# Performance work log

Hardware: AMD Instinct MI355X
Metric: run time of the kernel (lower is better)

Reference implementation:

```python
import jax, jax.numpy as jnp
import numpy as np

B, T, D, NH, DK = 2, 2048, 1024, 16, 64
EPS = 1e-6

def proj_H(z):
    return z - z.mean(axis=-1, keepdims=True)

def to_clr(p):
    return proj_H(jnp.log(p + EPS))

def setup_inputs() -> dict:
    key = jax.random.key(0)
    ks = jax.random.split(key, 9)
    p = jax.random.uniform(ks[0], (B, T, D), dtype=jnp.float32)
    # xavier_uniform with gain=0.8 for square-ish [in,out] matrices
    def xavier(k, fan_in, fan_out):
        bound = 0.8 * np.sqrt(6.0 / (fan_in + fan_out))
        return jax.random.uniform(k, (fan_in, fan_out), minval=-bound, maxval=bound, dtype=jnp.float32)
    H = NH * DK
    Wq = xavier(ks[1], D, H); bq = jnp.zeros((H,), jnp.float32)
    Wk = xavier(ks[2], D, H); bk = jnp.zeros((H,), jnp.float32)
    Wv = xavier(ks[3], D, H); bv = jnp.zeros((H,), jnp.float32)
    Wo = xavier(ks[4], H, D); bo = jnp.zeros((D,), jnp.float32)
    return {"p": p, "Wq": Wq, "bq": bq, "Wk": Wk, "bk": bk,
            "Wv": Wv, "bv": bv, "Wo": Wo, "bo": bo}

def reference(p, Wq, bq, Wk, bk, Wv, bv, Wo, bo):
    z = to_clr(p)                                   # [B,T,D]
    # projections with H-projection epilogue, reshaped to [B,T,NH,DK]
    q = proj_H(z @ Wq + bq).reshape(B, T, NH, DK)
    k = proj_H(z @ Wk + bk).reshape(B, T, NH, DK)
    v = proj_H(z @ Wv + bv).reshape(B, T, NH, DK)
    att = jnp.einsum('bihd,bjhd->bhij', q, k) / jnp.sqrt(jnp.float32(DK))
    w = jax.nn.softmax(att, axis=-1)                # dropout is identity in eval
    z_out = jnp.einsum('bhij,bjhd->bihd', w, v).reshape(B, T, NH * DK)
    z_out = proj_H(z_out @ Wo + bo)
    return jax.nn.softmax(z_out, axis=-1)           # from_clr
```

## Files before the change

### kernel.cpp

```cpp
#include <hip/hip_runtime.h>

typedef unsigned short u16;
typedef __attribute__((ext_vector_type(8))) short short8_t;
typedef __attribute__((ext_vector_type(4))) float f32x4;
typedef __attribute__((ext_vector_type(16))) float f32x16;
typedef __attribute__((ext_vector_type(4))) int int4v;
typedef __attribute__((ext_vector_type(2))) int int2v;

#define BB    2
#define TT    2048
#define DD    1024
#define NHEAD 16
#define DKH   64
#define HH    1024
#define MR    4096
#define CLR_EPS 1e-6f
#define QSCALE_CONST 0.18033688011112042f

#define O_WQKVT  0ull
#define O_WOT    6291456ull
#define O_WMEAN  8388608ull
#define O_BQKV   8404992ull
#define O_BO     8417280ull
#define O_Z      8421376ull
#define O_QKV    16809984ull
#define O_VT     41975808ull
#define O_ZOUT   50364416ull
#define O_LOGITS O_QKV

__device__ __forceinline__ u16 f2bf(float f) {
  unsigned u = __builtin_bit_cast(unsigned, f);
  u += 0x7FFFu + ((u >> 16) & 1u);
  return (u16)(u >> 16);
}
__device__ __forceinline__ float bf2f(u16 x) {
  unsigned u = ((unsigned)x) << 16;
  return __builtin_bit_cast(float, u);
}

typedef const __attribute__((address_space(1))) unsigned int as1_u32_t;
typedef __attribute__((address_space(3))) unsigned int as3_u32_t;

__device__ __forceinline__ void async16(const void* g, void* l) {
  __builtin_amdgcn_global_load_lds((as1_u32_t*)g, (as3_u32_t*)l, 16, 0, 0);
}

__global__ __launch_bounds__(256) void wprep_mean(
    const float* __restrict__ Wq, const float* __restrict__ Wk,
    const float* __restrict__ Wv, const float* __restrict__ Wo,
    const float* __restrict__ bq, const float* __restrict__ bk,
    const float* __restrict__ bv, const float* __restrict__ bo,
    float* __restrict__ wmean, float* __restrict__ bqkv_p, float* __restrict__ bo_p) {
  __shared__ float sb[4];
  const int bid = blockIdx.x, tid = threadIdx.x;
  if (bid < 4096) {
    const int m = bid >> 10, d = bid & 1023;
    const float* Wm = (m == 0) ? Wq : (m == 1) ? Wk : (m == 2) ? Wv : Wo;
    float4 x = ((const float4*)(Wm + (size_t)d * 1024))[tid];
    float s = x.x + x.y + x.z + x.w;
    #pragma unroll
    for (int dd = 32; dd; dd >>= 1) s += __shfl_xor(s, dd);
    if ((tid & 63) == 0) sb[tid >> 6] = s;
    __syncthreads();
    if (tid == 0) wmean[bid] = (sb[0] + sb[1] + sb[2] + sb[3]) * (1.f / 1024.f);
  } else {
    const int j = bid - 4096;
    const float* bb = (j == 0) ? bq : (j == 1) ? bk : (j == 2) ? bv : bo;
    float4 x = ((const float4*)bb)[tid];
    float s = x.x + x.y + x.z + x.w;
    #pragma unroll
    for (int dd = 32; dd; dd >>= 1) s += __shfl_xor(s, dd);
    if ((tid & 63) == 0) sb[tid >> 6] = s;
    __syncthreads();
    const float mean = (sb[0] + sb[1] + sb[2] + sb[3]) * (1.f / 1024.f);
    float* dst = (j < 3) ? (bqkv_p + j * 1024) : bo_p;
    float4 o = {x.x - mean, x.y - mean, x.z - mean, x.w - mean};
    ((float4*)dst)[tid] = o;
  }
}

__global__ __launch_bounds__(256) void wprep_trans(
    const float* __restrict__ Wq, const float* __restrict__ Wk,
    const float* __restrict__ Wv, const float* __restrict__ Wo,
    const float* __restrict__ wmean, u16* __restrict__ wqkvt, u16* __restrict__ wot) {
  __shared__ float tl[64][65];
  const int tj = blockIdx.x, ti = blockIdx.y, m = blockIdx.z;
  const int tid = threadIdx.x;
  const float* Wm = (m == 0) ? Wq : (m == 1) ? Wk : (m == 2) ? Wv : Wo;
  const int d0 = ti * 64, h0 = tj * 64;
  #pragma unroll
  for (int rr = 0; rr < 4; ++rr) {
    const int r = (tid >> 4) + rr * 16;
    float4 x = *(const float4*)(Wm + (size_t)(d0 + r) * 1024 + h0 + ((tid & 15) << 2));
    const float mu = wmean[m * 1024 + d0 + r];
    tl[r][(tid & 15) * 4 + 0] = x.x - mu;
    tl[r][(tid & 15) * 4 + 1] = x.y - mu;
    tl[r][(tid & 15) * 4 + 2] = x.z - mu;
    tl[r][(tid & 15) * 4 + 3] = x.w - mu;
  }
  __syncthreads();
  #pragma unroll
  for (int rr = 0; rr < 2; ++rr) {
    const int hh = (tid >> 3) + rr * 32;
    const int cd = (tid & 7) << 3;
    short8_t v;
    #pragma unroll
    for (int i = 0; i < 8; ++i) v[i] = (short)f2bf(tl[cd + i][hh]);
    u16* dst = (m < 3) ? (wqkvt + ((size_t)(m * 1024 + h0 + hh)) * 1024 + d0 + cd)
                       : (wot + ((size_t)(h0 + hh)) * 1024 + d0 + cd);
    *(short8_t*)dst = v;
  }
}

__global__ __launch_bounds__(256) void clr_kernel(const float* __restrict__ p, u16* __restrict__ z) {
  __shared__ float sb[4];
  const int r = blockIdx.x, tid = threadIdx.x;
  float4 x = ((const float4*)(p + (size_t)r * 1024))[tid];
  float l0 = __logf(x.x + CLR_EPS), l1 = __logf(x.y + CLR_EPS);
  float l2 = __logf(x.z + CLR_EPS), l3 = __logf(x.w + CLR_EPS);
  float s = l0 + l1 + l2 + l3;
  #pragma unroll
  for (int dd = 32; dd; dd >>= 1) s += __shfl_xor(s, dd);
  if ((tid & 63) == 0) sb[tid >> 6] = s;
  __syncthreads();
  const float mu = (sb[0] + sb[1] + sb[2] + sb[3]) * (1.f / 1024.f);
  ushort4 o;
  o.x = f2bf(l0 - mu); o.y = f2bf(l1 - mu); o.z = f2bf(l2 - mu); o.w = f2bf(l3 - mu);
  ((ushort4*)(z + (size_t)r * 1024))[tid] = o;
}

template <bool OUTF32, bool QSC>
__global__ __launch_bounds__(256) void gemm_bt(
    const u16* __restrict__ A, const u16* __restrict__ Bt, const float* __restrict__ bias,
    void* __restrict__ Cout, int Ndim, int Kdim) {
  __shared__ u16 As[128 * 64];
  __shared__ u16 Bs[128 * 64];
  const int tid = threadIdx.x;
  const int lane = tid & 63, wid = tid >> 6;
  const int m0 = blockIdx.y * 128, n0 = blockIdx.x * 128;
  const int wm = wid >> 1, wn = wid & 1;
  const int srow = tid >> 3, schk = tid & 7;
  f32x4 acc[4][4] = {};

  for (int k0 = 0; k0 < Kdim; k0 += 64) {
    __syncthreads();
    #pragma unroll
    for (int rr = 0; rr < 4; ++rr) {
      const int row = srow + rr * 32;
      const int gcol = k0 + ((schk ^ (row & 7)) << 3);
      async16(A + (size_t)(m0 + row) * Kdim + gcol, &As[row * 64 + schk * 8]);
      async16(Bt + (size_t)(n0 + row) * Kdim + gcol, &Bs[row * 64 + schk * 8]);
    }
    __syncthreads();
    #pragma unroll
    for (int kk = 0; kk < 64; kk += 32) {
      short8_t af[4], bf[4];
      #pragma unroll
      for (int i = 0; i < 4; ++i) {
        const int arow = wm * 64 + i * 16 + (lane & 15);
        const int abyte = (arow * 128 + ((kk + ((lane >> 4) << 3)) << 1)) ^ ((arow & 7) << 4);
        af[i] = *(const short8_t*)((const char*)As + abyte);
        const int brow = wn * 64 + i * 16 + (lane & 15);
        const int bbyte = (brow * 128 + ((kk + ((lane >> 4) << 3)) << 1)) ^ ((brow & 7) << 4);
        bf[i] = *(const short8_t*)((const char*)Bs + bbyte);
      }
      #pragma unroll
      for (int i = 0; i < 4; ++i)
        #pragma unroll
        for (int j = 0; j < 4; ++j)
          acc[i][j] = __builtin_amdgcn_mfma_f32_16x16x32_bf16(af[i], bf[j], acc[i][j], 0, 0, 0);
    }
  }
  #pragma unroll
  for (int j = 0; j < 4; ++j) {
    const int col = n0 + wn * 64 + j * 16 + (lane & 15);
    const float bb = bias[col];
    const float sc = (QSC && col < 1024) ? QSCALE_CONST : 1.0f;
    #pragma unroll
    for (int i = 0; i < 4; ++i) {
      const int rowb = m0 + wm * 64 + i * 16 + ((lane >> 4) << 2);
      #pragma unroll
      for (int r = 0; r < 4; ++r) {
        const float v = (acc[i][j][r] + bb) * sc;
        if (OUTF32) ((float*)Cout)[(size_t)(rowb + r) * Ndim + col] = v;
        else        ((u16*)Cout)[(size_t)(rowb + r) * Ndim + col] = f2bf(v);
      }
    }
  }
}

__global__ __launch_bounds__(256) void vtrans(const u16* __restrict__ qkv, u16* __restrict__ vt) {
  __shared__ u16 tile[64][72];
  const int tt = blockIdx.x, h = blockIdx.y, b = blockIdx.z;
  const int tid = threadIdx.x;
  #pragma unroll
  for (int rr = 0; rr < 2; ++rr) {
    const int row = (tid >> 3) + rr * 32;
    const u16* src = qkv + (size_t)(b * TT + tt * 64 + row) * 3072 + 2048 + h * 64 + ((tid & 7) << 3);
    *(short8_t*)&tile[row][(tid & 7) << 3] = *(const short8_t*)src;
  }
  __syncthreads();
  #pragma unroll
  for (int rr = 0; rr < 2; ++rr) {
    const int dk = (tid >> 3) + rr * 32;
    const int t0 = (tid & 7) << 3;
    short8_t v;
    #pragma unroll
    for (int i = 0; i < 8; ++i) v[i] = (short)tile[t0 + i][dk];
    u16* dst = vt + ((size_t)(b * NHEAD + h) * 64 + dk) * (size_t)TT + tt * 64 + t0;
    *(short8_t*)dst = v;
  }
}

__global__ __launch_bounds__(512, 2) void attn_kernel(
    const u16* __restrict__ qkv, const u16* __restrict__ vt, u16* __restrict__ zout) {
  __shared__ char smem[65536];
  const int qb = blockIdx.x, h = blockIdx.y, b = blockIdx.z;
  const int tid = threadIdx.x, lane = tid & 63, w = tid >> 6;
  const int qw = w & 3, ks = w >> 2;
  const int hl = lane >> 5, l31 = lane & 31;
  const int swz = (l31 & 7) << 4;
  const int q0 = qb * 256 + qw * 64;

  short8_t qf[2][4];
  #pragma unroll
  for (int qt = 0; qt < 2; ++qt)
    #pragma unroll
    for (int c = 0; c < 4; ++c)
      qf[qt][c] = *(const short8_t*)(qkv + (size_t)(b * TT + q0 + qt * 32 + l31) * 3072
                                     + h * 64 + c * 16 + hl * 8);

  const int sr0 = qw * 16 + (lane >> 3);
  const int schk = lane & 7;
  const int scol = (schk ^ (sr0 & 7)) << 3;
  const int dof = sr0 * 128 + schk * 16;
  char* kls = smem + ks * 16384;
  char* vls = smem + 32768 + ks * 16384;
  const u16* kg = qkv + 1024 + (size_t)h * 64;
  const u16* vg = vt + (size_t)(b * NHEAD + h) * 64 * (size_t)TT;

  {
    const int kbase = ks * 1024;
    async16(kg + (size_t)(b * TT + kbase + sr0) * 3072 + scol, kls + dof);
    async16(kg + (size_t)(b * TT + kbase + sr0 + 8) * 3072 + scol, kls + dof + 1024);
    async16(vg + (size_t)sr0 * TT + kbase + scol, vls + dof);
    async16(vg + (size_t)(sr0 + 8) * TT + kbase + scol, vls + dof + 1024);
  }

  f32x16 o[2][2] = {};
  f32x16 lb[2] = {};
  short8_t ones;
  #pragma unroll
  for (int i = 0; i < 8; ++i) ones[i] = (short)0x3F80;

  for (int it = 0; it < 16; ++it) {
    __syncthreads();
    if (it < 15) {
      const int kbase = ks * 1024 + (it + 1) * 64;
      const int bo = ((it + 1) & 1) * 8192;
      async16(kg + (size_t)(b * TT + kbase + sr0) * 3072 + scol, kls + bo + dof);
      async16(kg + (size_t)(b * TT + kbase + sr0 + 8) * 3072 + scol, kls + bo + dof + 1024);
      async16(vg + (size_t)sr0 * TT + kbase + scol, vls + bo + dof);
      async16(vg + (size_t)(sr0 + 8) * TT + kbase + scol, vls + bo + dof + 1024);
    }
    const char* Kb = kls + (it & 1) * 8192;
    const char* Vb = vls + (it & 1) * 8192;

    #pragma unroll
    for (int kt = 0; kt < 2; ++kt) {
      f32x16 s[2] = {};
      #pragma unroll
      for (int c = 0; c < 4; ++c) {
        const int krow = kt * 32 + l31;
        const short8_t kfr = *(const short8_t*)(Kb + krow * 128 + ((c * 32 + hl * 16) ^ swz));
        s[0] = __builtin_amdgcn_mfma_f32_32x32x16_bf16(kfr, qf[0][c], s[0], 0, 0, 0);
        s[1] = __builtin_amdgcn_mfma_f32_32x32x16_bf16(kfr, qf[1][c], s[1], 0, 0, 0);
      }
      #pragma unroll
      for (int qt = 0; qt < 2; ++qt)
        #pragma unroll
        for (int r = 0; r < 16; ++r) {
          float pv;
          asm("v_exp_f32 %0, %1" : "=v"(pv) : "v"(s[qt][r]));
          s[qt][r] = pv;
        }
      #pragma unroll
      for (int cc = 0; cc < 2; ++cc) {
        short8_t pa[2];
        #pragma unroll
        for (int qt = 0; qt < 2; ++qt) {
          int w0, w1, w2, w3;
          asm("v_cvt_pk_bf16_f32 %0, %1, %2" : "=v"(w0) : "v"(s[qt][8 * cc + 0]), "v"(s[qt][8 * cc + 1]));
          asm("v_cvt_pk_bf16_f32 %0, %1, %2" : "=v"(w1) : "v"(s[qt][8 * cc + 2]), "v"(s[qt][8 * cc + 3]));
          asm("v_cvt_pk_bf16_f32 %0, %1, %2" : "=v"(w2) : "v"(s[qt][8 * cc + 4]), "v"(s[qt][8 * cc + 5]));
          asm("v_cvt_pk_bf16_f32 %0, %1, %2" : "=v"(w3) : "v"(s[qt][8 * cc + 6]), "v"(s[qt][8 * cc + 7]));
          int4v fw = {w0, w1, w2, w3};
          pa[qt] = __builtin_bit_cast(short8_t, fw);
          lb[qt] = __builtin_amdgcn_mfma_f32_32x32x16_bf16(pa[qt], ones, lb[qt], 0, 0, 0);
        }
        const int cb0 = 64 * kt + 32 * cc + 8 * hl;
        #pragma unroll
        for (int dkt = 0; dkt < 2; ++dkt) {
          const int vrow = dkt * 32 + l31;
          const int2v d0 = *(const int2v*)(Vb + vrow * 128 + (cb0 ^ swz));
          const int2v d1 = *(const int2v*)(Vb + vrow * 128 + ((cb0 + 16) ^ swz));
          int4v vv = {d0.x, d0.y, d1.x, d1.y};
          const short8_t vfr = __builtin_bit_cast(short8_t, vv);
          o[0][dkt] = __builtin_amdgcn_mfma_f32_32x32x16_bf16(pa[0], vfr, o[0][dkt], 0, 0, 0);
          o[1][dkt] = __builtin_amdgcn_mfma_f32_32x32x16_bf16(pa[1], vfr, o[1][dkt], 0, 0, 0);
        }
      }
    }
  }

  __syncthreads();
  const int slot = qw * 64 + lane;
  if (ks == 1) {
    u16* ro = (u16*)(smem + slot * 136);
    #pragma unroll
    for (int qt = 0; qt < 2; ++qt)
      #pragma unroll
      for (int dkt = 0; dkt < 2; ++dkt)
        #pragma unroll
        for (int r = 0; r < 16; ++r)
          ro[(qt * 2 + dkt) * 16 + r] = f2bf(o[qt][dkt][r]);
    u16* rl = (u16*)(smem + 36864 + slot * 72);
    #pragma unroll
    for (int qt = 0; qt < 2; ++qt)
      #pragma unroll
      for (int r = 0; r < 16; ++r)
        rl[qt * 16 + r] = f2bf(lb[qt][r]);
  }
  __syncthreads();
  if (ks == 0) {
    const u16* ro = (const u16*)(smem + slot * 136);
    const u16* rl = (const u16*)(smem + 36864 + slot * 72);
    #pragma unroll
    for (int qt = 0; qt < 2; ++qt) {
      #pragma unroll
      for (int r = 0; r < 16; ++r) lb[qt][r] += bf2f(rl[qt * 16 + r]);
      #pragma unroll
      for (int dkt = 0; dkt < 2; ++dkt)
        #pragma unroll
        for (int r = 0; r < 16; ++r) o[qt][dkt][r] += bf2f(ro[(qt * 2 + dkt) * 16 + r]);
    }
    #pragma unroll
    for (int qt = 0; qt < 2; ++qt) {
      float rlv[16];
      #pragma unroll
      for (int r = 0; r < 16; ++r) rlv[r] = 1.f / lb[qt][r];
      #pragma unroll
      for (int dkt = 0; dkt < 2; ++dkt) {
        const int col = h * 64 + dkt * 32 + l31;
        #pragma unroll
        for (int r = 0; r < 16; ++r) {
          const int rowg = b * TT + q0 + qt * 32 + (r & 3) + 8 * (r >> 2) + 4 * hl;
          zout[(size_t)rowg * 1024 + col] = f2bf(o[qt][dkt][r] * rlv[r]);
        }
      }
    }
  }
}

__global__ __launch_bounds__(256) void softmax_rows(const float* __restrict__ logits,
                                                    float* __restrict__ out) {
  __shared__ float sb[8];
  const int r = blockIdx.x, tid = threadIdx.x;
  float4 x = ((const float4*)(logits + (size_t)r * 1024))[tid];
  float mx = fmaxf(fmaxf(x.x, x.y), fmaxf(x.z, x.w));
  #pragma unroll
  for (int dd = 32; dd; dd >>= 1) mx = fmaxf(mx, __shfl_xor(mx, dd));
  if ((tid & 63) == 0) sb[tid >> 6] = mx;
  __syncthreads();
  mx = fmaxf(fmaxf(sb[0], sb[1]), fmaxf(sb[2], sb[3]));
  const float e0 = __expf(x.x - mx), e1 = __expf(x.y - mx);
  const float e2 = __expf(x.z - mx), e3 = __expf(x.w - mx);
  float s = e0 + e1 + e2 + e3;
  #pragma unroll
  for (int dd = 32; dd; dd >>= 1) s += __shfl_xor(s, dd);
  __syncthreads();
  if ((tid & 63) == 0) sb[4 + (tid >> 6)] = s;
  __syncthreads();
  s = sb[4] + sb[5] + sb[6] + sb[7];
  const float inv = 1.f / s;
  float4 o = {e0 * inv, e1 * inv, e2 * inv, e3 * inv};
  ((float4*)(out + (size_t)r * 1024))[tid] = o;
}

extern "C" void kernel_launch(void* const* d_in, const int* in_sizes, int n_in,
                              void* d_out, int out_size, void* d_ws, size_t ws_size,
                              hipStream_t stream) {
  (void)in_sizes; (void)n_in; (void)out_size; (void)ws_size;
  const float* p  = (const float*)d_in[0];
  const float* Wq = (const float*)d_in[1];
  const float* bq = (const float*)d_in[2];
  const float* Wk = (const float*)d_in[3];
  const float* bk = (const float*)d_in[4];
  const float* Wv = (const float*)d_in[5];
  const float* bv = (const float*)d_in[6];
  const float* Wo = (const float*)d_in[7];
  const float* bo = (const float*)d_in[8];
  float* out = (float*)d_out;

  char* ws = (char*)d_ws;
  u16*   wqkvt  = (u16*)(ws + O_WQKVT);
  u16*   wot    = (u16*)(ws + O_WOT);
  float* wmean  = (float*)(ws + O_WMEAN);
  float* bqkv_p = (float*)(ws + O_BQKV);
  float* bo_p   = (float*)(ws + O_BO);
  u16*   z      = (u16*)(ws + O_Z);
  u16*   qkv    = (u16*)(ws + O_QKV);
  u16*   vt     = (u16*)(ws + O_VT);
  u16*   zoutb  = (u16*)(ws + O_ZOUT);
  float* logits = (float*)(ws + O_LOGITS);

  wprep_mean<<<4100, 256, 0, stream>>>(Wq, Wk, Wv, Wo, bq, bk, bv, bo, wmean, bqkv_p, bo_p);
  wprep_trans<<<dim3(16, 16, 4), 256, 0, stream>>>(Wq, Wk, Wv, Wo, wmean, wqkvt, wot);
  clr_kernel<<<MR, 256, 0, stream>>>(p, z);
  gemm_bt<false, true><<<dim3(3072 / 128, MR / 128), 256, 0, stream>>>(z, wqkvt, bqkv_p, qkv, 3072, 1024);
  vtrans<<<dim3(TT / 64, NHEAD, BB), 256, 0, stream>>>(qkv, vt);
  attn_kernel<<<dim3(TT / 256, NHEAD, BB), 512, 0, stream>>>(qkv, vt, zoutb);
  gemm_bt<true, false><<<dim3(1024 / 128, MR / 128), 256, 0, stream>>>(zoutb, wot, bo_p, logits, 1024, 1024);
  softmax_rows<<<MR, 256, 0, stream>>>(logits, out);
}
```

Baseline: 139.4 us.

## Replace QKV GEMM with 256x256 double-buffered phased kernel and fuse V transpose

```diff
diff --git a/kernel.cpp b/kernel.cpp
--- a/kernel.cpp
+++ b/kernel.cpp
@@ -43,6 +43,19 @@
 
 __device__ __forceinline__ void async16(const void* g, void* l) {
   __builtin_amdgcn_global_load_lds((as1_u32_t*)g, (as3_u32_t*)l, 16, 0, 0);
+}
+
+__device__ __forceinline__ void stage2(const u16* __restrict__ G, int base_row,
+                                       int r0, int r1, int k0, int schk, u16* lds) {
+  const int c0 = k0 + ((schk ^ (r0 & 7)) << 3);
+  const int c1 = k0 + ((schk ^ (r1 & 7)) << 3);
+  async16(G + (size_t)(base_row + r0) * 1024 + c0, lds + r0 * 64 + schk * 8);
+  async16(G + (size_t)(base_row + r1) * 1024 + c1, lds + r1 * 64 + schk * 8);
+}
+
+__device__ __forceinline__ short8_t ldfrag(const u16* buf, int row, int kh, int lane) {
+  const int byte = (row * 128 + ((kh * 32 + ((lane >> 4) << 3)) << 1)) ^ ((row & 7) << 4);
+  return *(const short8_t*)((const char*)buf + byte);
 }
 
 __global__ __launch_bounds__(256) void wprep_mean(
@@ -129,10 +142,143 @@
   ((ushort4*)(z + (size_t)r * 1024))[tid] = o;
 }
 
-template <bool OUTF32, bool QSC>
+__global__ __launch_bounds__(512, 2) void gemm_qkv_8ph(
+    const u16* __restrict__ A, const u16* __restrict__ Bt, const float* __restrict__ bias,
+    u16* __restrict__ qkv, u16* __restrict__ vt) {
+  __shared__ u16 As[2][256 * 64];
+  __shared__ u16 Bs[2][256 * 64];
+  const int tid = threadIdx.x, lane = tid & 63, wid = tid >> 6;
+  const int wm = wid >> 2, wn = wid & 3;
+  const int id = blockIdx.x;
+  const int nid = (id & 7) * 24 + (id >> 3);
+  const int m0 = (nid / 12) * 256, n0 = (nid % 12) * 256;
+  const int srow = tid >> 3, schk = tid & 7;
+  const int l15 = lane & 15, lg4 = (lane >> 4) << 2;
+
+  f32x4 acc[8][4] = {};
+
+  stage2(Bt, n0, srow, srow + 64, 0, schk, &Bs[0][0]);
+  stage2(Bt, n0, srow + 128, srow + 192, 0, schk, &Bs[0][0]);
+  stage2(A, m0, srow, srow + 128, 0, schk, &As[0][0]);
+  stage2(A, m0, srow + 64, srow + 192, 0, schk, &As[0][0]);
+  asm volatile("s_waitcnt vmcnt(2)" ::: "memory");
+  __builtin_amdgcn_s_barrier();
+
+  short8_t afr[4], bfr[4];
+  for (int t = 0; t < 16; ++t) {
+    const int cur = t & 1;
+    const int k0n = ((t + 1) & 15) * 64;
+    const u16* Ab = &As[cur][0];
+    const u16* Bb_ = &Bs[cur][0];
+    u16* Asn = &As[cur ^ 1][0];
+    u16* Bsn = &Bs[cur ^ 1][0];
+
+    #pragma unroll
+    for (int j = 0; j < 4; ++j) bfr[j] = ldfrag(Bb_, wn * 64 + j * 16 + l15, 0, lane);
+    #pragma unroll
+    for (int i = 0; i < 4; ++i) afr[i] = ldfrag(Ab, wm * 128 + i * 16 + l15, 0, lane);
+    stage2(Bt, n0, srow, srow + 64, k0n, schk, Bsn);
+    asm volatile("s_waitcnt vmcnt(2)" ::: "memory");
+    __builtin_amdgcn_s_barrier();
+    asm volatile("s_waitcnt lgkmcnt(0)" ::: "memory");
+    __builtin_amdgcn_sched_barrier(0);
+    __builtin_amdgcn_s_setprio(1);
+    #pragma unroll
+    for (int i = 0; i < 4; ++i)
+      #pragma unroll
+      for (int j = 0; j < 4; ++j)
+        acc[i][j] = __builtin_amdgcn_mfma_f32_16x16x32_bf16(afr[i], bfr[j], acc[i][j], 0, 0, 0);
+    __builtin_amdgcn_s_setprio(0);
+    __builtin_amdgcn_s_barrier();
+
+    #pragma unroll
+    for (int i = 0; i < 4; ++i) afr[i] = ldfrag(Ab, wm * 128 + 64 + i * 16 + l15, 0, lane);
+    stage2(Bt, n0, srow + 128, srow + 192, k0n, schk, Bsn);
+    __builtin_amdgcn_s_barrier();
+    asm volatile("s_waitcnt lgkmcnt(0)" ::: "memory");
+    __builtin_amdgcn_sched_barrier(0);
+    __builtin_amdgcn_s_setprio(1);
+    #pragma unroll
+    for (int i = 0; i < 4; ++i)
+      #pragma unroll
+      for (int j = 0; j < 4; ++j)
+        acc[4 + i][j] = __builtin_amdgcn_mfma_f32_16x16x32_bf16(afr[i], bfr[j], acc[4 + i][j], 0, 0, 0);
+    __builtin_amdgcn_s_setprio(0);
+    __builtin_amdgcn_s_barrier();
+
+    #pragma unroll
+    for (int j = 0; j < 4; ++j) bfr[j] = ldfrag(Bb_, wn * 64 + j * 16 + l15, 1, lane);
+    #pragma unroll
+    for (int i = 0; i < 4; ++i) afr[i] = ldfrag(Ab, wm * 128 + i * 16 + l15, 1, lane);
+    stage2(A, m0, srow, srow + 128, k0n, schk, Asn);
+    __builtin_amdgcn_s_barrier();
+    asm volatile("s_waitcnt lgkmcnt(0)" ::: "memory");
+    __builtin_amdgcn_sched_barrier(0);
+    __builtin_amdgcn_s_setprio(1);
+    #pragma unroll
+    for (int i = 0; i < 4; ++i)
+      #pragma unroll
+      for (int j = 0; j < 4; ++j)
+        acc[i][j] = __builtin_amdgcn_mfma_f32_16x16x32_bf16(afr[i], bfr[j], acc[i][j], 0, 0, 0);
+    __builtin_amdgcn_s_setprio(0);
+    __builtin_amdgcn_s_barrier();
+
+    #pragma unroll
+    for (int i = 0; i < 4; ++i) afr[i] = ldfrag(Ab, wm * 128 + 64 + i * 16 + l15, 1, lane);
+    stage2(A, m0, srow + 64, srow + 192, k0n, schk, Asn);
+    asm volatile("s_waitcnt vmcnt(2)" ::: "memory");
+    __builtin_amdgcn_s_barrier();
+    asm volatile("s_waitcnt lgkmcnt(0)" ::: "memory");
+    __builtin_amdgcn_sched_barrier(0);
+    __builtin_amdgcn_s_setprio(1);
+    #pragma unroll
+    for (int i = 0; i < 4; ++i)
+      #pragma unroll
+      for (int j = 0; j < 4; ++j)
+        acc[4 + i][j] = __builtin_amdgcn_mfma_f32_16x16x32_bf16(afr[i], bfr[j], acc[4 + i][j], 0, 0, 0);
+    __builtin_amdgcn_s_setprio(0);
+    __builtin_amdgcn_s_barrier();
+  }
+  asm volatile("s_waitcnt vmcnt(0)" ::: "memory");
+
+  if (n0 < 2048) {
+    const float sc = (n0 < 1024) ? QSCALE_CONST : 1.0f;
+    #pragma unroll
+    for (int j = 0; j < 4; ++j) {
+      const int col = n0 + wn * 64 + j * 16 + l15;
+      const float bb = bias[col];
+      #pragma unroll
+      for (int i = 0; i < 8; ++i) {
+        const int rowb = m0 + wm * 128 + i * 16 + lg4;
+        #pragma unroll
+        for (int r = 0; r < 4; ++r)
+          qkv[(size_t)(rowb + r) * 3072 + col] = f2bf((acc[i][j][r] + bb) * sc);
+      }
+    }
+  } else {
+    const int h = (n0 - 2048 + wn * 64) >> 6;
+    #pragma unroll
+    for (int j = 0; j < 4; ++j) {
+      const int dk = j * 16 + l15;
+      const float bb = bias[n0 + wn * 64 + dk];
+      #pragma unroll
+      for (int i = 0; i < 8; ++i) {
+        const int rowb = m0 + wm * 128 + i * 16 + lg4;
+        const int b = rowb >> 11, tq = rowb & 2047;
+        ushort4 pk;
+        pk.x = f2bf(acc[i][j][0] + bb);
+        pk.y = f2bf(acc[i][j][1] + bb);
+        pk.z = f2bf(acc[i][j][2] + bb);
+        pk.w = f2bf(acc[i][j][3] + bb);
+        *(ushort4*)(vt + ((size_t)((b * NHEAD + h) * 64 + dk)) * TT + tq) = pk;
+      }
+    }
+  }
+}
+
 __global__ __launch_bounds__(256) void gemm_bt(
     const u16* __restrict__ A, const u16* __restrict__ Bt, const float* __restrict__ bias,
-    void* __restrict__ Cout, int Ndim, int Kdim) {
+    float* __restrict__ Cout, int Ndim, int Kdim) {
   __shared__ u16 As[128 * 64];
   __shared__ u16 Bs[128 * 64];
   const int tid = threadIdx.x;
@@ -153,16 +299,12 @@
     }
     __syncthreads();
     #pragma unroll
-    for (int kk = 0; kk < 64; kk += 32) {
+    for (int kk = 0; kk < 2; ++kk) {
       short8_t af[4], bf[4];
       #pragma unroll
       for (int i = 0; i < 4; ++i) {
-        const int arow = wm * 64 + i * 16 + (lane & 15);
-        const int abyte = (arow * 128 + ((kk + ((lane >> 4) << 3)) << 1)) ^ ((arow & 7) << 4);
-        af[i] = *(const short8_t*)((const char*)As + abyte);
-        const int brow = wn * 64 + i * 16 + (lane & 15);
-        const int bbyte = (brow * 128 + ((kk + ((lane >> 4) << 3)) << 1)) ^ ((brow & 7) << 4);
-        bf[i] = *(const short8_t*)((const char*)Bs + bbyte);
+        af[i] = ldfrag(As, wm * 64 + i * 16 + (lane & 15), kk, lane);
+        bf[i] = ldfrag(Bs, wn * 64 + i * 16 + (lane & 15), kk, lane);
       }
       #pragma unroll
       for (int i = 0; i < 4; ++i)
@@ -175,40 +317,13 @@
   for (int j = 0; j < 4; ++j) {
     const int col = n0 + wn * 64 + j * 16 + (lane & 15);
     const float bb = bias[col];
-    const float sc = (QSC && col < 1024) ? QSCALE_CONST : 1.0f;
     #pragma unroll
     for (int i = 0; i < 4; ++i) {
       const int rowb = m0 + wm * 64 + i * 16 + ((lane >> 4) << 2);
       #pragma unroll
-      for (int r = 0; r < 4; ++r) {
-        const float v = (acc[i][j][r] + bb) * sc;
-        if (OUTF32) ((float*)Cout)[(size_t)(rowb + r) * Ndim + col] = v;
-        else        ((u16*)Cout)[(size_t)(rowb + r) * Ndim + col] = f2bf(v);
-      }
-    }
-  }
-}
-
-__global__ __launch_bounds__(256) void vtrans(const u16* __restrict__ qkv, u16* __restrict__ vt) {
-  __shared__ u16 tile[64][72];
-  const int tt = blockIdx.x, h = blockIdx.y, b = blockIdx.z;
-  const int tid = threadIdx.x;
-  #pragma unroll
-  for (int rr = 0; rr < 2; ++rr) {
-    const int row = (tid >> 3) + rr * 32;
-    const u16* src = qkv + (size_t)(b * TT + tt * 64 + row) * 3072 + 2048 + h * 64 + ((tid & 7) << 3);
-    *(short8_t*)&tile[row][(tid & 7) << 3] = *(const short8_t*)src;
-  }
-  __syncthreads();
-  #pragma unroll
-  for (int rr = 0; rr < 2; ++rr) {
-    const int dk = (tid >> 3) + rr * 32;
-    const int t0 = (tid & 7) << 3;
-    short8_t v;
-    #pragma unroll
-    for (int i = 0; i < 8; ++i) v[i] = (short)tile[t0 + i][dk];
-    u16* dst = vt + ((size_t)(b * NHEAD + h) * 64 + dk) * (size_t)TT + tt * 64 + t0;
-    *(short8_t*)dst = v;
+      for (int r = 0; r < 4; ++r)
+        Cout[(size_t)(rowb + r) * Ndim + col] = acc[i][j][r] + bb;
+    }
   }
 }
 
@@ -417,9 +532,8 @@
   wprep_mean<<<4100, 256, 0, stream>>>(Wq, Wk, Wv, Wo, bq, bk, bv, bo, wmean, bqkv_p, bo_p);
   wprep_trans<<<dim3(16, 16, 4), 256, 0, stream>>>(Wq, Wk, Wv, Wo, wmean, wqkvt, wot);
   clr_kernel<<<MR, 256, 0, stream>>>(p, z);
-  gemm_bt<false, true><<<dim3(3072 / 128, MR / 128), 256, 0, stream>>>(z, wqkvt, bqkv_p, qkv, 3072, 1024);
-  vtrans<<<dim3(TT / 64, NHEAD, BB), 256, 0, stream>>>(qkv, vt);
+  gemm_qkv_8ph<<<192, 512, 0, stream>>>(z, wqkvt, bqkv_p, qkv, vt);
   attn_kernel<<<dim3(TT / 256, NHEAD, BB), 512, 0, stream>>>(qkv, vt, zoutb);
-  gemm_bt<true, false><<<dim3(1024 / 128, MR / 128), 256, 0, stream>>>(zoutb, wot, bo_p, logits, 1024, 1024);
+  gemm_bt<<<dim3(1024 / 128, MR / 128), 256, 0, stream>>>(zoutb, wot, bo_p, logits, 1024, 1024);
   softmax_rows<<<MR, 256, 0, stream>>>(logits, out);
 }
```

Result: faster. 132.6 us (-4.9%).
